# Performance work log

Measured on AMD Instinct MI355X. Metric: run time of the kernel, lower is better.

The kernel has to match this reference:

```python
import jax, jax.numpy as jnp
import numpy as np

H = 1024      # hidden_size
NH = 16       # num_heads
DK = H // NH  # head dim


def setup_inputs() -> dict:
    key = jax.random.key(0)
    ks = jax.random.split(key, 5)
    s = 0.02
    return {
        "x": jax.random.normal(ks[0], (4, 2048, H), dtype=jnp.float32),
        "W_attn": jax.random.normal(ks[1], (H, 3 * H), dtype=jnp.float32) * s,
        "b_attn": jnp.zeros((3 * H,), dtype=jnp.float32),
        "W_proj": jax.random.normal(ks[2], (H, H), dtype=jnp.float32) * s,
        "b_proj": jnp.zeros((H,), dtype=jnp.float32),
    }


def reference(x, W_attn, b_attn, W_proj, b_proj):
    B, S, _ = x.shape
    qkv = x @ W_attn + b_attn                      # [B,S,3H]
    q, k, v = jnp.split(qkv, 3, axis=-1)
    # split heads -> [B,NH,S,DK]
    def heads(t):
        return t.reshape(B, S, NH, DK).transpose(0, 2, 1, 3)
    q, k, v = heads(q), heads(k), heads(v)
    scores = jnp.einsum("bhqd,bhkd->bhqk", q, k) / jnp.sqrt(jnp.float32(DK))
    causal = jnp.triu(jnp.full((S, S), -jnp.inf, dtype=scores.dtype), k=1)
    scores = scores + causal                        # additive causal mask
    attn = jax.nn.softmax(scores, axis=-1)
    out = jnp.einsum("bhqk,bhkd->bhqd", attn, v)   # [B,NH,S,DK]
    out = out.transpose(0, 2, 1, 3).reshape(B, S, H)
    return out @ W_proj + b_proj
```

## Files before the change

### kernel.cpp

```cpp
#include <hip/hip_runtime.h>
#include <hip/hip_bf16.h>


typedef __attribute__((ext_vector_type(8))) short bhalf8;
typedef __attribute__((ext_vector_type(4))) float floatx4;
typedef __attribute__((ext_vector_type(16))) float floatx16;

#define SB 2048
#define HB 1024
#define H3 3072

#if __has_builtin(__builtin_amdgcn_exp2f)
#define EXP2(x) __builtin_amdgcn_exp2f(x)
#else
#define EXP2(x) exp2f(x)
#endif

__device__ __forceinline__ float bf2f(unsigned short u) {
  union { unsigned int i; float f; } c; c.i = ((unsigned int)u) << 16; return c.f;
}
__device__ __forceinline__ unsigned short f2bf(float f) {
  union { float f; unsigned int i; } c; c.f = f;
  unsigned int r = c.i + 0x7fffu + ((c.i >> 16) & 1u);
  return (unsigned short)(r >> 16);
}
__device__ __forceinline__ int pkbf(float lo, float hi_) {
  union { __hip_bfloat162 h; int i; } u;
  u.h = __float22bfloat162_rn(make_float2(lo, hi_));
  return u.i;
}

__device__ __forceinline__ void gl_lds16(const unsigned short* g, unsigned short* l) {
  __builtin_amdgcn_global_load_lds(
      (const __attribute__((address_space(1))) unsigned int*)g,
      (__attribute__((address_space(3))) unsigned int*)l, 16, 0, 0);
}

#define REP16(OP) OP(0) OP(1) OP(2) OP(3) OP(4) OP(5) OP(6) OP(7) \
                  OP(8) OP(9) OP(10) OP(11) OP(12) OP(13) OP(14) OP(15)

__global__ void cvt_f32_bf16(const float* __restrict__ in, unsigned short* __restrict__ out, int n) {
  int i = (blockIdx.x * blockDim.x + threadIdx.x) * 4;
  if (i >= n) return;
  float4 v = *(const float4*)(in + i);
  ushort4 o;
  o.x = f2bf(v.x); o.y = f2bf(v.y); o.z = f2bf(v.z); o.w = f2bf(v.w);
  *(ushort4*)(out + i) = o;
}

__global__ void transpose_cvt(const float* __restrict__ in, unsigned short* __restrict__ out,
                              int K, int N) {
  __shared__ float tile[32][33];
  int n0 = blockIdx.x * 32, k0 = blockIdx.y * 32;
  for (int i = threadIdx.y; i < 32; i += 8)
    tile[i][threadIdx.x] = in[(size_t)(k0 + i) * N + n0 + threadIdx.x];
  __syncthreads();
  for (int i = threadIdx.y; i < 32; i += 8)
    out[(size_t)(n0 + i) * K + k0 + threadIdx.x] = f2bf(tile[threadIdx.x][i]);
}

__global__ void transpose_v(const unsigned short* __restrict__ qkv,
                            unsigned short* __restrict__ Vt) {
  __shared__ unsigned short tile[32][33];
  const int bh = blockIdx.z;
  const int b = bh >> 4, h = bh & 15;
  const int s0 = blockIdx.x * 32;
  const int d0 = blockIdx.y * 32;
  const int tx = threadIdx.x;
  const unsigned short* src = qkv + (size_t)(b * SB + s0) * H3 + 2 * HB + h * 64 + d0;
  for (int i = threadIdx.y; i < 32; i += 8)
    tile[i][tx] = src[(size_t)i * H3 + tx];
  __syncthreads();
  unsigned short* dst = Vt + ((size_t)bh * 64 + d0) * SB + s0;
  for (int i = threadIdx.y; i < 32; i += 8)
    dst[(size_t)i * SB + tx] = tile[tx][i];
}

template <bool F32OUT>
__global__ __launch_bounds__(256, 3) void gemm_ring3(
    const unsigned short* __restrict__ A,
    const unsigned short* __restrict__ Bt,
    const float* __restrict__ bias,
    void* __restrict__ Cv,
    int M, int N, int K) {
  __shared__ __align__(16) unsigned short Sm[3 * 8192];
  const int tid = threadIdx.x;
  const int lane = tid & 63;
  const int w = tid >> 6;
  const int l15 = lane & 15, l4 = lane >> 4;

  const int gx = gridDim.x;
  int lin = blockIdx.y * gx + blockIdx.x;
  const int cpx = (gx * gridDim.y) >> 3;
  lin = (lin & 7) * cpx + (lin >> 3);
  const int m0 = (lin / gx) * 128;
  const int n0 = (lin % gx) * 128;
  const int wr = (w >> 1) * 64;
  const int wc = (w & 1) * 64;

  const int srow = tid >> 2;
  const int lch = ((tid & 3) ^ ((tid >> 3) & 3)) * 8;
  const unsigned short* pA = A + (size_t)(m0 + srow) * K + lch;
  const unsigned short* pB = Bt + (size_t)(n0 + srow) * K + lch;
  const size_t rK64 = (size_t)64 * K;

  int abyte[4], bbyte[4];
#pragma unroll
  for (int i = 0; i < 4; ++i) {
    int ra = wr + i * 16 + l15;
    abyte[i] = ra * 64 + ((l4 ^ ((ra >> 1) & 3)) << 4);
    int rb = wc + i * 16 + l15;
    bbyte[i] = 8192 + rb * 64 + ((l4 ^ ((rb >> 1) & 3)) << 4);
  }

  const floatx4 zero = {0.f, 0.f, 0.f, 0.f};
  floatx4 acc[4][4];
#pragma unroll
  for (int i = 0; i < 4; ++i)
#pragma unroll
    for (int j = 0; j < 4; ++j) acc[i][j] = zero;

#define STAGE_G(k0, sbase)                                              \
  { gl_lds16(pA + (k0),        Sm + (sbase) + tid * 8);                 \
    gl_lds16(pA + (k0) + rK64, Sm + (sbase) + 2048 + tid * 8);          \
    gl_lds16(pB + (k0),        Sm + (sbase) + 4096 + tid * 8);          \
    gl_lds16(pB + (k0) + rK64, Sm + (sbase) + 6144 + tid * 8); }

  const int NT = K >> 5;
  STAGE_G(0, 0)
  STAGE_G(32, 8192)
  int sb = 0;
  int ss = 16384;

  for (int t = 0; t < NT; ++t) {
    if (t < NT - 1) asm volatile("s_waitcnt vmcnt(4)" ::: "memory");
    else            asm volatile("s_waitcnt vmcnt(0)" ::: "memory");
    __builtin_amdgcn_s_barrier();

    const char* LB = (const char*)(Sm + sb);
    bhalf8 b0 = *(const bhalf8*)(LB + bbyte[0]);
    bhalf8 b1 = *(const bhalf8*)(LB + bbyte[1]);
    bhalf8 b2 = *(const bhalf8*)(LB + bbyte[2]);
    bhalf8 b3 = *(const bhalf8*)(LB + bbyte[3]);

    if (t + 2 < NT) STAGE_G((t + 2) * 32, ss)

    __builtin_amdgcn_s_setprio(1);
#pragma unroll
    for (int mi = 0; mi < 4; ++mi) {
      bhalf8 a = *(const bhalf8*)(LB + abyte[mi]);
      acc[mi][0] = __builtin_amdgcn_mfma_f32_16x16x32_bf16(a, b0, acc[mi][0], 0, 0, 0);
      acc[mi][1] = __builtin_amdgcn_mfma_f32_16x16x32_bf16(a, b1, acc[mi][1], 0, 0, 0);
      acc[mi][2] = __builtin_amdgcn_mfma_f32_16x16x32_bf16(a, b2, acc[mi][2], 0, 0, 0);
      acc[mi][3] = __builtin_amdgcn_mfma_f32_16x16x32_bf16(a, b3, acc[mi][3], 0, 0, 0);
    }
    __builtin_amdgcn_s_setprio(0);

    __builtin_amdgcn_sched_barrier(0);
    asm volatile("s_waitcnt lgkmcnt(0)" ::: "memory");
    __builtin_amdgcn_s_barrier();

    sb = (sb == 16384) ? 0 : sb + 8192;
    ss = (ss == 16384) ? 0 : ss + 8192;
  }
#undef STAGE_G

  float* Cf = (float*)Cv;
  unsigned short* Cb = (unsigned short*)Cv;
#pragma unroll
  for (int i = 0; i < 4; ++i) {
    int row = m0 + wr + i * 16 + (l4 << 2);
#pragma unroll
    for (int j = 0; j < 4; ++j) {
      int col = n0 + wc + j * 16 + l15;
      float bb = bias[col];
#pragma unroll
      for (int r = 0; r < 4; ++r) {
        float v = acc[i][j][r] + bb;
        size_t idx = (size_t)(row + r) * N + col;
        if constexpr (F32OUT) Cf[idx] = v;
        else Cb[idx] = f2bf(v);
      }
    }
  }
}

__global__ __launch_bounds__(256, 4) void flash_attn4(
    const unsigned short* __restrict__ qkv,
    const unsigned short* __restrict__ Vt,
    unsigned short* __restrict__ outp) {
  __shared__ __align__(16) unsigned short Sm[4 * 4096];

  const int tid = threadIdx.x;
  const int lane = tid & 63;
  const int w = tid >> 6;
  const int hi = lane >> 5;
  const int qc = lane & 31;
  const int bh = blockIdx.x;
  const int b = bh >> 4, h = bh & 15;
  const int qt = 15 - (int)blockIdx.y;
  const int wq0 = qt * 128 + w * 32;
  const size_t rowbase = (size_t)b * SB;
  const int qg = wq0 + qc;
  const int nt = 2 * qt + 2;

  bhalf8 qf[4];
  {
    const unsigned short* qp = qkv + (rowbase + qg) * H3 + h * 64 + hi * 8;
#pragma unroll
    for (int kk = 0; kk < 4; ++kk) {
      bhalf8 v = *(const bhalf8*)(qp + kk * 16);
      bhalf8 o;
#pragma unroll
      for (int j = 0; j < 8; ++j)
        o[j] = (short)f2bf(bf2f((unsigned short)v[j]) * 0.18033688f);
      qf[kk] = o;
    }
  }

  const floatx16 Z16 = {0,0,0,0,0,0,0,0,0,0,0,0,0,0,0,0};
  floatx16 acc0 = Z16, acc1 = Z16;
  float l_half = 0.f;

  const char* LB = (const char*)Sm;
  int koff[8];
#pragma unroll
  for (int kk = 0; kk < 4; ++kk) {
    int xo = (((2 * kk + hi) ^ (qc & 7)) << 4);
    koff[2 * kk]     = qc * 128 + xo;
    koff[2 * kk + 1] = (32 + qc) * 128 + xo;
  }

  const int srow = tid >> 3, schk = tid & 7;
  const int sxe = (schk ^ (srow & 7)) * 8;
  const unsigned short* kp = qkv + (rowbase + srow) * H3 + HB + h * 64 + sxe;
  const unsigned short* vp = Vt + ((size_t)bh * 64 + srow) * SB + sxe;

  {
    unsigned short* kb = Sm + tid * 8;
    gl_lds16(kp, kb);
    gl_lds16(kp + 32 * H3, kb + 2048);
    gl_lds16(vp, kb + 8192);
    gl_lds16(vp + 32 * SB, kb + 8192 + 2048);
  }

#define QKK(BUFB, kk)                                                              \
      { bhalf8 ka = *(const bhalf8*)(LB + (BUFB) + koff[2*(kk)]);                  \
        s0 = __builtin_amdgcn_mfma_f32_32x32x16_bf16(ka, qf[kk], s0, 0, 0, 0);     \
        bhalf8 kb2 = *(const bhalf8*)(LB + (BUFB) + koff[2*(kk)+1]);               \
        s1 = __builtin_amdgcn_mfma_f32_32x32x16_bf16(kb2, qf[kk], s1, 0, 0, 0); }
#define PVC(BUFB, c, pfv)                                                          \
      { bhalf8 va = *(const bhalf8*)(LB + 16384 + (BUFB) + koff[2*(c)]);           \
        acc0 = __builtin_amdgcn_mfma_f32_32x32x16_bf16(va, pfv, acc0, 0, 0, 0);    \
        bhalf8 vb2 = *(const bhalf8*)(LB + 16384 + (BUFB) + koff[2*(c)+1]);        \
        acc1 = __builtin_amdgcn_mfma_f32_32x32x16_bf16(vb2, pfv, acc1, 0, 0, 0); }
#define MSK0(r) { if (k0 + (((r)&3) + 8*((r)>>2)) + 4*hi > qg)      s0[r] = -3.0e38f; }
#define MSK1(r) { if (k0 + 32 + (((r)&3) + 8*((r)>>2)) + 4*hi > qg) s1[r] = -3.0e38f; }
#define PEXP(r) { s0[r] = EXP2(s0[r]); s1[r] = EXP2(s1[r]); rsx[(r)&3] += s0[r] + s1[r]; }
  union PW { int i[4]; bhalf8 v; };
#define PACK2(dst, sv, rb)                                               \
      { int A0 = pkbf(sv[rb + 0], sv[rb + 1]);                           \
        int A1 = pkbf(sv[rb + 2], sv[rb + 3]);                           \
        int B0 = pkbf(sv[rb + 4], sv[rb + 5]);                           \
        int B1 = pkbf(sv[rb + 6], sv[rb + 7]);                           \
        auto r0 = __builtin_amdgcn_permlane32_swap(A0, B0, false, false);\
        auto r1 = __builtin_amdgcn_permlane32_swap(A1, B1, false, false);\
        PW u;                                                            \
        u.i[0] = r0[0]; u.i[1] = r1[0];                                  \
        u.i[2] = r0[1]; u.i[3] = r1[1];                                  \
        dst = u.v; }

#define FLASH_COMPUTE(BUFB)                                                        \
    { floatx16 s0 = Z16, s1 = Z16;                                                 \
      __builtin_amdgcn_s_setprio(1);                                               \
      QKK(BUFB, 0) QKK(BUFB, 1) QKK(BUFB, 2) QKK(BUFB, 3)                          \
      __builtin_amdgcn_s_setprio(0);                                               \
      if (k0 + 63 > wq0) { REP16(MSK0) REP16(MSK1) }                               \
      float rsx[4] = {0.f, 0.f, 0.f, 0.f};                                         \
      REP16(PEXP)                                                                  \
      l_half += (rsx[0] + rsx[1]) + (rsx[2] + rsx[3]);                             \
      bhalf8 pf0, pf1, pf2, pf3;                                                   \
      PACK2(pf0, s0, 0) PACK2(pf1, s0, 8) PACK2(pf2, s1, 0) PACK2(pf3, s1, 8)      \
      __builtin_amdgcn_s_setprio(1);                                               \
      PVC(BUFB, 0, pf0) PVC(BUFB, 1, pf1) PVC(BUFB, 2, pf2) PVC(BUFB, 3, pf3)      \
      __builtin_amdgcn_s_setprio(0); }

#define DO_STEP(T, BUF)                                                            \
  { __syncthreads();                                                               \
    if ((T) + 1 < nt) {                                                            \
      kp += 64 * H3; vp += 64;                                                     \
      unsigned short* kb = Sm + (1 - (BUF)) * 4096 + tid * 8;                      \
      gl_lds16(kp, kb); gl_lds16(kp + 32 * H3, kb + 2048);                         \
      gl_lds16(vp, kb + 8192); gl_lds16(vp + 32 * SB, kb + 8192 + 2048);           \
    }                                                                              \
    const int k0 = (T) * 64;                                                       \
    if (k0 <= wq0 + 31) FLASH_COMPUTE((BUF) * 8192)                                \
  }

  for (int t = 0; t < nt; t += 2) {
    DO_STEP(t, 0)
    DO_STEP(t + 1, 1)
  }

  const float l_full = l_half + __shfl_xor(l_half, 32);
  const float inv_l = 1.f / l_full;
  unsigned short* op = outp + (rowbase + qg) * HB + h * 64;
#pragma unroll
  for (int tq = 0; tq < 4; ++tq) {
    ushort4 st;
    st.x = f2bf(acc0[4 * tq + 0] * inv_l);
    st.y = f2bf(acc0[4 * tq + 1] * inv_l);
    st.z = f2bf(acc0[4 * tq + 2] * inv_l);
    st.w = f2bf(acc0[4 * tq + 3] * inv_l);
    *(ushort4*)(op + 8 * tq + 4 * hi) = st;
    ushort4 su;
    su.x = f2bf(acc1[4 * tq + 0] * inv_l);
    su.y = f2bf(acc1[4 * tq + 1] * inv_l);
    su.z = f2bf(acc1[4 * tq + 2] * inv_l);
    su.w = f2bf(acc1[4 * tq + 3] * inv_l);
    *(ushort4*)(op + 32 + 8 * tq + 4 * hi) = su;
  }
}

extern "C" void kernel_launch(void* const* d_in, const int* in_sizes, int n_in,
                              void* d_out, int out_size, void* d_ws, size_t ws_size,
                              hipStream_t stream) {
  const float* x      = (const float*)d_in[0];
  const float* W_attn = (const float*)d_in[1];
  const float* b_attn = (const float*)d_in[2];
  const float* W_proj = (const float*)d_in[3];
  const float* b_proj = (const float*)d_in[4];
  float* out = (float*)d_out;

  char* ws = (char*)d_ws;
  unsigned short* x_bf    = (unsigned short*)(ws);
  unsigned short* Wt_attn = (unsigned short*)(ws + 16777216);
  unsigned short* Wt_proj = (unsigned short*)(ws + 23068672);
  unsigned short* qkv     = (unsigned short*)(ws + 25165824);
  unsigned short* attn    = (unsigned short*)(ws + 75497472);
  unsigned short* Vt      = x_bf;

  cvt_f32_bf16<<<8192, 256, 0, stream>>>(x, x_bf, 8192 * 1024);
  transpose_cvt<<<dim3(96, 32), dim3(32, 8), 0, stream>>>(W_attn, Wt_attn, 1024, 3072);
  transpose_cvt<<<dim3(32, 32), dim3(32, 8), 0, stream>>>(W_proj, Wt_proj, 1024, 1024);

  gemm_ring3<false><<<dim3(24, 64), 256, 0, stream>>>(x_bf, Wt_attn, b_attn, qkv,
                                                      8192, 3072, 1024);
  transpose_v<<<dim3(64, 2, 64), dim3(32, 8), 0, stream>>>(qkv, Vt);
  flash_attn4<<<dim3(64, 16), 256, 0, stream>>>(qkv, Vt, attn);
  gemm_ring3<true><<<dim3(8, 64), 256, 0, stream>>>(attn, Wt_proj, b_proj, out,
                                                    8192, 1024, 1024);
}
```

Measured before the change: 166.8 us.

## Enlarge GEMM tiles to 256x128 with 8 waves and split-phase staging

Replaces the 128x128, 4-wave GEMM with a 256x128 tile computed by 8 waves (512 threads), so each B tile in LDS is reused across twice as many rows. The main loop is split into two MFMA halves separated by barriers, with A staging issued before the first half and B staging before the second, which interleaves global-to-LDS loads with compute. LDS per block grows to 72 KB and the grid halves, which reduces occupancy and adds an extra barrier per K step.

```diff
diff --git a/kernel.cpp b/kernel.cpp
--- a/kernel.cpp
+++ b/kernel.cpp
@@ -77,32 +77,31 @@
 }
 
 template <bool F32OUT>
-__global__ __launch_bounds__(256, 3) void gemm_ring3(
+__global__ __launch_bounds__(512, 4) void gemm_v6(
     const unsigned short* __restrict__ A,
     const unsigned short* __restrict__ Bt,
     const float* __restrict__ bias,
     void* __restrict__ Cv,
     int M, int N, int K) {
-  __shared__ __align__(16) unsigned short Sm[3 * 8192];
+  __shared__ __align__(16) unsigned short Sm[3 * 12288];
   const int tid = threadIdx.x;
   const int lane = tid & 63;
   const int w = tid >> 6;
   const int l15 = lane & 15, l4 = lane >> 4;
+  const int wr = (w >> 1) * 64;
+  const int wc = (w & 1) * 64;
 
   const int gx = gridDim.x;
   int lin = blockIdx.y * gx + blockIdx.x;
   const int cpx = (gx * gridDim.y) >> 3;
   lin = (lin & 7) * cpx + (lin >> 3);
-  const int m0 = (lin / gx) * 128;
+  const int m0 = (lin / gx) * 256;
   const int n0 = (lin % gx) * 128;
-  const int wr = (w >> 1) * 64;
-  const int wc = (w & 1) * 64;
-
-  const int srow = tid >> 2;
-  const int lch = ((tid & 3) ^ ((tid >> 3) & 3)) * 8;
-  const unsigned short* pA = A + (size_t)(m0 + srow) * K + lch;
-  const unsigned short* pB = Bt + (size_t)(n0 + srow) * K + lch;
-  const size_t rK64 = (size_t)64 * K;
+
+  const int idx0 = tid, idx1 = tid + 512;
+  const unsigned short* pA0 = A + (size_t)(m0 + (idx0 >> 2)) * K + (((idx0 & 3) ^ ((idx0 >> 3) & 3)) * 8);
+  const unsigned short* pA1 = A + (size_t)(m0 + (idx1 >> 2)) * K + (((idx1 & 3) ^ ((idx1 >> 3) & 3)) * 8);
+  const unsigned short* pB  = Bt + (size_t)(n0 + (tid >> 2)) * K + (((tid & 3) ^ ((tid >> 3) & 3)) * 8);
 
   int abyte[4], bbyte[4];
 #pragma unroll
@@ -110,7 +109,7 @@
     int ra = wr + i * 16 + l15;
     abyte[i] = ra * 64 + ((l4 ^ ((ra >> 1) & 3)) << 4);
     int rb = wc + i * 16 + l15;
-    bbyte[i] = 8192 + rb * 64 + ((l4 ^ ((rb >> 1) & 3)) << 4);
+    bbyte[i] = 16384 + rb * 64 + ((l4 ^ ((rb >> 1) & 3)) << 4);
   }
 
   const floatx4 zero = {0.f, 0.f, 0.f, 0.f};
@@ -120,50 +119,72 @@
 #pragma unroll
     for (int j = 0; j < 4; ++j) acc[i][j] = zero;
 
-#define STAGE_G(k0, sbase)                                              \
-  { gl_lds16(pA + (k0),        Sm + (sbase) + tid * 8);                 \
-    gl_lds16(pA + (k0) + rK64, Sm + (sbase) + 2048 + tid * 8);          \
-    gl_lds16(pB + (k0),        Sm + (sbase) + 4096 + tid * 8);          \
-    gl_lds16(pB + (k0) + rK64, Sm + (sbase) + 6144 + tid * 8); }
+#define STAGE_A(k0, sbase)                                              \
+  { gl_lds16(pA0 + (k0), Sm + (sbase) + idx0 * 8);                      \
+    gl_lds16(pA1 + (k0), Sm + (sbase) + idx1 * 8); }
+#define STAGE_B(k0, sbase)                                              \
+  { gl_lds16(pB + (k0), Sm + (sbase) + 8192 + tid * 8); }
 
   const int NT = K >> 5;
-  STAGE_G(0, 0)
-  STAGE_G(32, 8192)
+  STAGE_A(0, 0)  STAGE_B(0, 0)
+  STAGE_A(32, 12288) STAGE_B(32, 12288)
   int sb = 0;
-  int ss = 16384;
+  int ss = 24576;
 
   for (int t = 0; t < NT; ++t) {
-    if (t < NT - 1) asm volatile("s_waitcnt vmcnt(4)" ::: "memory");
+    if (t < NT - 1) asm volatile("s_waitcnt vmcnt(3)" ::: "memory");
     else            asm volatile("s_waitcnt vmcnt(0)" ::: "memory");
     __builtin_amdgcn_s_barrier();
 
     const char* LB = (const char*)(Sm + sb);
+    const int k2 = (t + 2) * 32;
+    const bool st = (t + 2 < NT);
+
+    bhalf8 a0 = *(const bhalf8*)(LB + abyte[0]);
+    bhalf8 a1 = *(const bhalf8*)(LB + abyte[1]);
     bhalf8 b0 = *(const bhalf8*)(LB + bbyte[0]);
     bhalf8 b1 = *(const bhalf8*)(LB + bbyte[1]);
     bhalf8 b2 = *(const bhalf8*)(LB + bbyte[2]);
     bhalf8 b3 = *(const bhalf8*)(LB + bbyte[3]);
-
-    if (t + 2 < NT) STAGE_G((t + 2) * 32, ss)
-
+    if (st) STAGE_A(k2, ss)
+    asm volatile("s_waitcnt lgkmcnt(0)" ::: "memory");
+    __builtin_amdgcn_sched_barrier(0);
     __builtin_amdgcn_s_setprio(1);
-#pragma unroll
-    for (int mi = 0; mi < 4; ++mi) {
-      bhalf8 a = *(const bhalf8*)(LB + abyte[mi]);
-      acc[mi][0] = __builtin_amdgcn_mfma_f32_16x16x32_bf16(a, b0, acc[mi][0], 0, 0, 0);
-      acc[mi][1] = __builtin_amdgcn_mfma_f32_16x16x32_bf16(a, b1, acc[mi][1], 0, 0, 0);
-      acc[mi][2] = __builtin_amdgcn_mfma_f32_16x16x32_bf16(a, b2, acc[mi][2], 0, 0, 0);
-      acc[mi][3] = __builtin_amdgcn_mfma_f32_16x16x32_bf16(a, b3, acc[mi][3], 0, 0, 0);
-    }
+    acc[0][0] = __builtin_amdgcn_mfma_f32_16x16x32_bf16(a0, b0, acc[0][0], 0, 0, 0);
+    acc[0][1] = __builtin_amdgcn_mfma_f32_16x16x32_bf16(a0, b1, acc[0][1], 0, 0, 0);
+    acc[0][2] = __builtin_amdgcn_mfma_f32_16x16x32_bf16(a0, b2, acc[0][2], 0, 0, 0);
+    acc[0][3] = __builtin_amdgcn_mfma_f32_16x16x32_bf16(a0, b3, acc[0][3], 0, 0, 0);
+    acc[1][0] = __builtin_amdgcn_mfma_f32_16x16x32_bf16(a1, b0, acc[1][0], 0, 0, 0);
+    acc[1][1] = __builtin_amdgcn_mfma_f32_16x16x32_bf16(a1, b1, acc[1][1], 0, 0, 0);
+    acc[1][2] = __builtin_amdgcn_mfma_f32_16x16x32_bf16(a1, b2, acc[1][2], 0, 0, 0);
+    acc[1][3] = __builtin_amdgcn_mfma_f32_16x16x32_bf16(a1, b3, acc[1][3], 0, 0, 0);
     __builtin_amdgcn_s_setprio(0);
-
     __builtin_amdgcn_sched_barrier(0);
+    __builtin_amdgcn_s_barrier();
+
+    bhalf8 a2 = *(const bhalf8*)(LB + abyte[2]);
+    bhalf8 a3 = *(const bhalf8*)(LB + abyte[3]);
+    if (st) STAGE_B(k2, ss)
     asm volatile("s_waitcnt lgkmcnt(0)" ::: "memory");
+    __builtin_amdgcn_sched_barrier(0);
+    __builtin_amdgcn_s_setprio(1);
+    acc[2][0] = __builtin_amdgcn_mfma_f32_16x16x32_bf16(a2, b0, acc[2][0], 0, 0, 0);
+    acc[2][1] = __builtin_amdgcn_mfma_f32_16x16x32_bf16(a2, b1, acc[2][1], 0, 0, 0);
+    acc[2][2] = __builtin_amdgcn_mfma_f32_16x16x32_bf16(a2, b2, acc[2][2], 0, 0, 0);
+    acc[2][3] = __builtin_amdgcn_mfma_f32_16x16x32_bf16(a2, b3, acc[2][3], 0, 0, 0);
+    acc[3][0] = __builtin_amdgcn_mfma_f32_16x16x32_bf16(a3, b0, acc[3][0], 0, 0, 0);
+    acc[3][1] = __builtin_amdgcn_mfma_f32_16x16x32_bf16(a3, b1, acc[3][1], 0, 0, 0);
+    acc[3][2] = __builtin_amdgcn_mfma_f32_16x16x32_bf16(a3, b2, acc[3][2], 0, 0, 0);
+    acc[3][3] = __builtin_amdgcn_mfma_f32_16x16x32_bf16(a3, b3, acc[3][3], 0, 0, 0);
+    __builtin_amdgcn_s_setprio(0);
+    __builtin_amdgcn_sched_barrier(0);
     __builtin_amdgcn_s_barrier();
 
-    sb = (sb == 16384) ? 0 : sb + 8192;
-    ss = (ss == 16384) ? 0 : ss + 8192;
-  }
-#undef STAGE_G
+    sb = (sb == 24576) ? 0 : sb + 12288;
+    ss = (ss == 24576) ? 0 : ss + 12288;
+  }
+#undef STAGE_A
+#undef STAGE_B
 
   float* Cf = (float*)Cv;
   unsigned short* Cb = (unsigned short*)Cv;
@@ -344,10 +365,10 @@
   transpose_cvt<<<dim3(96, 32), dim3(32, 8), 0, stream>>>(W_attn, Wt_attn, 1024, 3072);
   transpose_cvt<<<dim3(32, 32), dim3(32, 8), 0, stream>>>(W_proj, Wt_proj, 1024, 1024);
 
-  gemm_ring3<false><<<dim3(24, 64), 256, 0, stream>>>(x_bf, Wt_attn, b_attn, qkv,
-                                                      8192, 3072, 1024);
+  gemm_v6<false><<<dim3(24, 32), 512, 0, stream>>>(x_bf, Wt_attn, b_attn, qkv,
+                                                   8192, 3072, 1024);
   transpose_v<<<dim3(64, 2, 64), dim3(32, 8), 0, stream>>>(qkv, Vt);
   flash_attn4<<<dim3(64, 16), 256, 0, stream>>>(qkv, Vt, attn);
-  gemm_ring3<true><<<dim3(8, 64), 256, 0, stream>>>(attn, Wt_proj, b_proj, out,
-                                                    8192, 1024, 1024);
-}
+  gemm_v6<true><<<dim3(8, 32), 512, 0, stream>>>(attn, Wt_proj, b_proj, out,
+                                                 8192, 1024, 1024);
+}
```

New measurement: 158.5 us. 5.0% less time.
